# Performance work log

Hardware: AMD Instinct MI355X
Metric: run time of the kernel (lower is better)

The kernel has to match this reference:

```python
import jax, jax.numpy as jnp
import numpy as np

# Node feature layout used by gridfm-graphkit: [Pd, Qd, Pg, Qg, Vm, Va]
PD, QD, PG, QG, VM, VA = 0, 1, 2, 3, 4, 5

N_NODES = 2_000_000
N_EDGES = 32_000_000
N_FEAT = 6


def setup_inputs() -> dict:
    key = jax.random.key(0)
    k1, k2, k3, k4, k5 = jax.random.split(key, 5)
    pred = jax.random.normal(k1, (N_NODES, N_FEAT), dtype=jnp.float32)
    target = jax.random.normal(k2, (N_NODES, N_FEAT), dtype=jnp.float32)
    edge_attr = jax.random.normal(k3, (N_EDGES, 2), dtype=jnp.float32)  # (G, B)
    edge_index = jax.random.randint(k4, (2, N_EDGES), 0, N_NODES, dtype=jnp.int64)
    mask = jax.random.randint(k5, (N_NODES, N_FEAT), 0, 2) > 0  # True -> use prediction
    return {"pred": pred, "target": target, "edge_attr": edge_attr,
            "edge_index": edge_index, "mask": mask}


def _power_flow_residual(pred, target, edge_attr, edge_index, mask):
    # Use prediction where the value was masked, ground truth elsewhere.
    x = jnp.where(mask, pred, target)  # [N, 6]
    # Complex bus voltage V = Vm * exp(i Va)
    V = (x[:, VM] * jnp.exp(1j * x[:, VA])).astype(jnp.complex64)  # [N]
    # Complex admittance per edge (Ybus entry)
    Y = (edge_attr[:, 0] + 1j * edge_attr[:, 1]).astype(jnp.complex64)  # [E]
    src, dst = edge_index[0], edge_index[1]
    # PyG MessagePassing (source_to_target, aggr='add'):
    # I_i = sum_{e: dst(e)=i} Y_e * V_{src(e)}
    msgs = Y * V[src]  # [E] complex, gather on src
    I = jax.ops.segment_sum(msgs, dst, num_segments=pred.shape[0])  # [N] complex
    # Net injected complex power S = (Pg - Pd) + j (Qg - Qd)
    Sbus = (x[:, PG] - x[:, PD]) + 1j * (x[:, QG] - x[:, QD])
    # Power-flow residual: S - V * conj(I)
    return Sbus - V * jnp.conj(I)  # [N] complex64


def reference(pred, target, edge_attr, edge_index, mask):
    residual = _power_flow_residual(pred, target, edge_attr, edge_index, mask)
    loss = jnp.mean(jnp.abs(residual))
    real_loss = jnp.mean(jnp.abs(jnp.real(residual)))
    imag_loss = jnp.mean(jnp.abs(jnp.imag(residual)))
    # Matches {'loss', 'Active Power Loss', 'Reactive Power Loss'} of PBELoss
    return jnp.stack([loss, real_loss, imag_loss])
```

## Files before the change

### kernel.cpp

```cpp
#include <hip/hip_runtime.h>
#include <hip/hip_fp16.h>
#include <math.h>


#define PBE_NT     256
#define PBE_NB     512
#define PBE_BSHIFT 12
#define PBE_BSIZE  4096
#define PBE_TILE   4096
#define PBE_NTB    512
#define PBE_EPT    (PBE_TILE / PBE_NTB)

#define PBE_SCALE64       2097152.0f
#define PBE_INV_SCALE64   (1.0f / 2097152.0f)
#define PBE_SCALE_LDS     524288.0f
#define PBE_INV_SCALE_LDS (1.0f / 524288.0f)

typedef unsigned long long ull;
typedef int iv4 __attribute__((ext_vector_type(4)));
union H2U { __half2 h; unsigned u; };

__device__ __forceinline__ float2 ld_nt_f2(const float2* p) {
    double d = __builtin_nontemporal_load(reinterpret_cast<const double*>(p));
    union { double d; float2 f; } u; u.d = d;
    return u.f;
}
__device__ __forceinline__ int ld_nt_i(const int* p) {
    return __builtin_nontemporal_load(p);
}
__device__ __forceinline__ int2 ld_nt_i2(const int* p) {
    long long v = __builtin_nontemporal_load(reinterpret_cast<const long long*>(p));
    int2 r; r.x = (int)(unsigned)(v & 0xFFFFFFFFll); r.y = (int)(v >> 32);
    return r;
}
__device__ __forceinline__ iv4 ld_nt_iv4(const int* p) {
    return __builtin_nontemporal_load(reinterpret_cast<const iv4*>(p));
}

__global__ void pbe_node_prep(const float* __restrict__ pred,
                              const float* __restrict__ target,
                              const int* __restrict__ mask,
                              float* __restrict__ V,
                              float* __restrict__ S,
                              unsigned* __restrict__ Vh,
                              int n) {
    int i = blockIdx.x * blockDim.x + threadIdx.x;
    int stride = gridDim.x * blockDim.x;
    for (; i < n; i += stride) {
        int b = 6 * i;
        float2 p0 = ld_nt_f2((const float2*)(pred + b));
        float2 p1 = ld_nt_f2((const float2*)(pred + b + 2));
        float2 p2 = ld_nt_f2((const float2*)(pred + b + 4));
        float2 t0 = ld_nt_f2((const float2*)(target + b));
        float2 t1 = ld_nt_f2((const float2*)(target + b + 2));
        float2 t2 = ld_nt_f2((const float2*)(target + b + 4));
        int2 m0 = ld_nt_i2(mask + b);
        int2 m1 = ld_nt_i2(mask + b + 2);
        int2 m2 = ld_nt_i2(mask + b + 4);
        float pd = m0.x ? p0.x : t0.x;
        float qd = m0.y ? p0.y : t0.y;
        float pg = m1.x ? p1.x : t1.x;
        float qg = m1.y ? p1.y : t1.y;
        float vm = m2.x ? p2.x : t2.x;
        float va = m2.y ? p2.y : t2.y;
        float sn, cs;
        sincosf(va, &sn, &cs);
        float vr = vm * cs, vi = vm * sn;
        V[2 * i + 0] = vr;
        V[2 * i + 1] = vi;
        S[2 * i + 0] = pg - pd;
        S[2 * i + 1] = qg - qd;
        if (Vh) { H2U u; u.h = __floats2half2_rn(vr, vi); Vh[i] = u.u; }
    }
}

__global__ void pbe_hist(const int* __restrict__ dst,
                         unsigned* __restrict__ hist_g, int e_total) {
    __shared__ unsigned h[PBE_NB];
    for (int b = threadIdx.x; b < PBE_NB; b += blockDim.x) h[b] = 0;
    __syncthreads();
    int n4 = e_total >> 2;
    int i = blockIdx.x * blockDim.x + threadIdx.x;
    int stride = gridDim.x * blockDim.x;
    for (; i < n4; i += stride) {
        iv4 v = ld_nt_iv4(dst + 4 * i);
        atomicAdd(&h[((unsigned)v[0]) >> PBE_BSHIFT], 1u);
        atomicAdd(&h[((unsigned)v[1]) >> PBE_BSHIFT], 1u);
        atomicAdd(&h[((unsigned)v[2]) >> PBE_BSHIFT], 1u);
        atomicAdd(&h[((unsigned)v[3]) >> PBE_BSHIFT], 1u);
    }
    if (blockIdx.x == 0) {
        for (int t = (n4 << 2) + threadIdx.x; t < e_total; t += blockDim.x)
            atomicAdd(&h[((unsigned)dst[t]) >> PBE_BSHIFT], 1u);
    }
    __syncthreads();
    for (int b = threadIdx.x; b < PBE_NB; b += blockDim.x)
        if (h[b]) atomicAdd(&hist_g[b], h[b]);
}

__global__ void pbe_prefix(const unsigned* __restrict__ hist_g,
                           unsigned* __restrict__ base,
                           unsigned* __restrict__ cursor) {
    __shared__ unsigned tmp[PBE_NB];
    int t = threadIdx.x;
    unsigned mine = hist_g[t];
    tmp[t] = mine;
    __syncthreads();
    for (int o = 1; o < PBE_NB; o <<= 1) {
        unsigned u = (t >= o) ? tmp[t - o] : 0u;
        __syncthreads();
        tmp[t] += u;
        __syncthreads();
    }
    unsigned excl = tmp[t] - mine;
    base[t] = excl;
    cursor[t] = excl;
}

__global__ void __launch_bounds__(PBE_NTB)
pbe_bin(const float2* __restrict__ Y,
        const int* __restrict__ src,
        const int* __restrict__ dst,
        const unsigned* __restrict__ Vh,
        ull* __restrict__ rec,
        unsigned* __restrict__ cursor,
        int e_total) {
    __shared__ unsigned hist[PBE_NB];
    __shared__ unsigned lbase[PBE_NB];
    __shared__ unsigned wsum[8];
    __shared__ unsigned staged_sh;
    __shared__ ull recs[PBE_TILE];

    const int tile0 = blockIdx.x * PBE_TILE;
    const int tid = threadIdx.x;
    hist[tid] = 0;
    __syncthreads();

    int d[PBE_EPT];
    #pragma unroll
    for (int k = 0; k < PBE_EPT; ++k) {
        int i = tile0 + k * PBE_NTB + tid;
        d[k] = (i < e_total) ? ld_nt_i(dst + i) : -1;
    }
    #pragma unroll
    for (int k = 0; k < PBE_EPT; ++k)
        if (d[k] >= 0) atomicAdd(&hist[((unsigned)d[k]) >> PBE_BSHIFT], 1u);
    __syncthreads();

    {
        unsigned mine = hist[tid];
        unsigned v = mine;
        #pragma unroll
        for (int o = 1; o < 64; o <<= 1) {
            unsigned u = __shfl_up(v, o);
            if ((tid & 63) >= o) v += u;
        }
        if ((tid & 63) == 63) wsum[tid >> 6] = v;
        __syncthreads();
        if (tid == 0) {
            unsigned acc = 0;
            #pragma unroll
            for (int wv = 0; wv < 8; ++wv) {
                unsigned t = wsum[wv]; wsum[wv] = acc; acc += t;
            }
        }
        __syncthreads();
        unsigned incl = v + wsum[tid >> 6];
        unsigned excl = incl - mine;
        lbase[tid] = excl;
        if (tid == PBE_NB - 1) staged_sh = incl;
        unsigned g = mine ? atomicAdd(&cursor[tid], mine) : 0u;
        hist[tid] = g - excl;
    }
    __syncthreads();

    #pragma unroll
    for (int h = 0; h < PBE_EPT / 8; ++h) {
        int s8[8]; unsigned uv[8]; float2 y8[8];
        #pragma unroll
        for (int j = 0; j < 8; ++j) {
            int k = h * 8 + j;
            int i = tile0 + k * PBE_NTB + tid;
            s8[j] = (d[k] >= 0) ? ld_nt_i(src + i) : 0;
        }
        #pragma unroll
        for (int j = 0; j < 8; ++j) uv[j] = Vh[s8[j]];
        #pragma unroll
        for (int j = 0; j < 8; ++j) {
            int k = h * 8 + j;
            int i = tile0 + k * PBE_NTB + tid;
            y8[j] = (d[k] >= 0) ? ld_nt_f2(Y + i) : make_float2(0.f, 0.f);
        }
        #pragma unroll
        for (int j = 0; j < 8; ++j) {
            int k = h * 8 + j;
            if (d[k] < 0) continue;
            unsigned b = ((unsigned)d[k]) >> PBE_BSHIFT;
            unsigned pos = atomicAdd(&lbase[b], 1u);
            H2U uvh; uvh.u = uv[j];
            float vr = __low2float(uvh.h), vi = __high2float(uvh.h);
            float mr = y8[j].x * vr - y8[j].y * vi;
            float mi = y8[j].x * vi + y8[j].y * vr;
            H2U um; um.h = __floats2half2_rn(mr, mi);
            recs[pos] = ((ull)b << 44)
                      | ((ull)(unsigned)(d[k] & (PBE_BSIZE - 1)) << 32)
                      | um.u;
        }
    }
    __syncthreads();

    unsigned staged = staged_sh;
    for (unsigned j = tid; j < staged; j += PBE_NTB) {
        ull r = recs[j];
        unsigned b = (unsigned)(r >> 44);
        __builtin_nontemporal_store(r & 0xFFFFFFFFFFFull, &rec[j + hist[b]]);
    }
}

__global__ void __launch_bounds__(512)
pbe_bucket_acc_red(const ull* __restrict__ rec,
                   const unsigned* __restrict__ base,
                   const unsigned* __restrict__ cursor,
                   const float* __restrict__ V,
                   const float* __restrict__ S,
                   float* __restrict__ sums, int n_nodes) {
    __shared__ int accR[PBE_BSIZE];
    __shared__ int accI[PBE_BSIZE];
    for (int j = threadIdx.x; j < PBE_BSIZE; j += 512) { accR[j] = 0; accI[j] = 0; }
    __syncthreads();
    const int b = blockIdx.x;
    const unsigned lo = base[b], hi = cursor[b];
    for (unsigned t = lo + threadIdx.x; t < hi; t += 512) {
        ull p = __builtin_nontemporal_load(rec + t);
        H2U um; um.u = (unsigned)p;
        unsigned dl = (unsigned)(p >> 32) & (PBE_BSIZE - 1);
        atomicAdd(&accR[dl], __float2int_rn(__low2float(um.h) * PBE_SCALE_LDS));
        atomicAdd(&accI[dl], __float2int_rn(__high2float(um.h) * PBE_SCALE_LDS));
    }
    __syncthreads();
    const int node0 = b << PBE_BSHIFT;
    float a0 = 0.f, a1 = 0.f, a2 = 0.f;
    for (int j = threadIdx.x; j < PBE_BSIZE; j += 512) {
        int n = node0 + j;
        if (n < n_nodes) {
            float2 v  = reinterpret_cast<const float2*>(V)[n];
            float2 sb = reinterpret_cast<const float2*>(S)[n];
            float cr = accR[j] * PBE_INV_SCALE_LDS;
            float ci = accI[j] * PBE_INV_SCALE_LDS;
            float rr = sb.x - (v.x * cr + v.y * ci);
            float ri = sb.y - (v.y * cr - v.x * ci);
            a0 += sqrtf(rr * rr + ri * ri);
            a1 += fabsf(rr);
            a2 += fabsf(ri);
        }
    }
    #pragma unroll
    for (int off = 32; off > 0; off >>= 1) {
        a0 += __shfl_down(a0, off);
        a1 += __shfl_down(a1, off);
        a2 += __shfl_down(a2, off);
    }
    __shared__ float sm[3][8];
    int wid  = threadIdx.x >> 6;
    int lane = threadIdx.x & 63;
    if (lane == 0) { sm[0][wid] = a0; sm[1][wid] = a1; sm[2][wid] = a2; }
    __syncthreads();
    if (threadIdx.x == 0) {
        float t0 = 0.f, t1 = 0.f, t2 = 0.f;
        #pragma unroll
        for (int wv = 0; wv < 8; ++wv) {
            t0 += sm[0][wv]; t1 += sm[1][wv]; t2 += sm[2][wv];
        }
        atomicAdd(&sums[0], t0);
        atomicAdd(&sums[1], t1);
        atomicAdd(&sums[2], t2);
    }
}

__device__ __forceinline__ void pbe_edge_one(float2 gb, int s, int d,
                                             const float2* __restrict__ V,
                                             ull* __restrict__ Iq) {
    float2 v = V[s];
    float mr = gb.x * v.x - gb.y * v.y;
    float mi = gb.x * v.y + gb.y * v.x;
    int qr = __float2int_rn(mr * PBE_SCALE64);
    int qi = __float2int_rn(mi * PBE_SCALE64);
    ull pack = ((ull)(unsigned)qr << 32) + (ull)(long long)qi;
    atomicAdd(&Iq[d], pack);
}

__global__ void __launch_bounds__(PBE_NT)
pbe_edge_scatter(const float2* __restrict__ edge_attr,
                 const int* __restrict__ src,
                 const int* __restrict__ dst,
                 const float2* __restrict__ V,
                 ull* __restrict__ Iq,
                 int e_total) {
    int i = blockIdx.x * blockDim.x + threadIdx.x;
    const int stride = gridDim.x * blockDim.x;
    for (; i + 3 * stride < e_total; i += 4 * stride) {
        int ia = i, ib = i + stride, ic = i + 2 * stride, id = i + 3 * stride;
        float2 ga = ld_nt_f2(edge_attr + ia);
        float2 gb = ld_nt_f2(edge_attr + ib);
        float2 gc = ld_nt_f2(edge_attr + ic);
        float2 gd = ld_nt_f2(edge_attr + id);
        int sa = ld_nt_i(src + ia), sb = ld_nt_i(src + ib);
        int sc = ld_nt_i(src + ic), sd = ld_nt_i(src + id);
        int da = ld_nt_i(dst + ia), db = ld_nt_i(dst + ib);
        int dc = ld_nt_i(dst + ic), dd = ld_nt_i(dst + id);
        pbe_edge_one(ga, sa, da, V, Iq);
        pbe_edge_one(gb, sb, db, V, Iq);
        pbe_edge_one(gc, sc, dc, V, Iq);
        pbe_edge_one(gd, sd, dd, V, Iq);
    }
    for (; i < e_total; i += stride) {
        float2 g = ld_nt_f2(edge_attr + i);
        pbe_edge_one(g, ld_nt_i(src + i), ld_nt_i(dst + i), V, Iq);
    }
}

__global__ void pbe_unpack_iq(ull* __restrict__ Iq, float* __restrict__ I, int n) {
    int i = blockIdx.x * blockDim.x + threadIdx.x;
    int stride = gridDim.x * blockDim.x;
    for (; i < n; i += stride) {
        long long q = (long long)Iq[i];
        int lo = (int)(unsigned)(q & 0xFFFFFFFFll);
        int hi = (int)((q - (long long)lo) >> 32);
        I[2 * i + 0] = hi * PBE_INV_SCALE64;
        I[2 * i + 1] = lo * PBE_INV_SCALE64;
    }
}

__global__ void pbe_reduce(const float* __restrict__ V,
                           const float* __restrict__ S,
                           const float* __restrict__ I,
                           float* __restrict__ sums, int n) {
    float a0 = 0.f, a1 = 0.f, a2 = 0.f;
    int i = blockIdx.x * blockDim.x + threadIdx.x;
    int stride = gridDim.x * blockDim.x;
    for (; i < n; i += stride) {
        float2 v  = reinterpret_cast<const float2*>(V)[i];
        float2 sb = reinterpret_cast<const float2*>(S)[i];
        float2 cc = reinterpret_cast<const float2*>(I)[i];
        float rr = sb.x - (v.x * cc.x + v.y * cc.y);
        float ri = sb.y - (v.y * cc.x - v.x * cc.y);
        a0 += sqrtf(rr * rr + ri * ri);
        a1 += fabsf(rr);
        a2 += fabsf(ri);
    }
    #pragma unroll
    for (int off = 32; off > 0; off >>= 1) {
        a0 += __shfl_down(a0, off);
        a1 += __shfl_down(a1, off);
        a2 += __shfl_down(a2, off);
    }
    __shared__ float sm[3][PBE_NT / 64];
    int wid  = threadIdx.x >> 6;
    int lane = threadIdx.x & 63;
    if (lane == 0) { sm[0][wid] = a0; sm[1][wid] = a1; sm[2][wid] = a2; }
    __syncthreads();
    if (threadIdx.x == 0) {
        float t0 = 0.f, t1 = 0.f, t2 = 0.f;
        #pragma unroll
        for (int w = 0; w < PBE_NT / 64; ++w) {
            t0 += sm[0][w]; t1 += sm[1][w]; t2 += sm[2][w];
        }
        atomicAdd(&sums[0], t0);
        atomicAdd(&sums[1], t1);
        atomicAdd(&sums[2], t2);
    }
}

__global__ void pbe_finalize(const float* __restrict__ sums,
                             float* __restrict__ out, float inv_n) {
    int t = threadIdx.x;
    if (t < 3) out[t] = sums[t] * inv_n;
}

static inline size_t align256(size_t x) { return (x + 255) & ~(size_t)255; }

extern "C" void kernel_launch(void* const* d_in, const int* in_sizes, int n_in,
                              void* d_out, int out_size, void* d_ws, size_t ws_size,
                              hipStream_t stream) {
    const float* pred      = (const float*)d_in[0];
    const float* target    = (const float*)d_in[1];
    const float* edge_attr = (const float*)d_in[2];
    const int*   edge_idx  = (const int*)d_in[3];
    const int*   mask      = (const int*)d_in[4];

    const int n_nodes = in_sizes[0] / 6;
    const int n_edges = in_sizes[2] / 2;
    const int* src = edge_idx;
    const int* dst = edge_idx + n_edges;

    const int NBa     = (n_nodes + PBE_BSIZE - 1) / PBE_BSIZE;
    const int n_tiles = (n_edges + PBE_TILE - 1) / PBE_TILE;

    char* w = (char*)d_ws;
    size_t oV    = 0;
    size_t oS    = align256(oV + (size_t)2 * n_nodes * 4);
    size_t oVh   = align256(oS + (size_t)2 * n_nodes * 4);
    size_t oRec  = align256(oVh + (size_t)n_nodes * 4);
    size_t oHist = align256(oRec + (size_t)n_edges * 8);
    size_t oBase = align256(oHist + PBE_NB * 4);
    size_t oCur  = align256(oBase + PBE_NB * 4);
    size_t oSums = align256(oCur + PBE_NB * 4);
    size_t need  = oSums + 3 * 4;

    float*    V      = (float*)(w + oV);
    float*    S      = (float*)(w + oS);
    unsigned* Vh     = (unsigned*)(w + oVh);
    ull*      rec    = (ull*)(w + oRec);
    unsigned* hist_g = (unsigned*)(w + oHist);
    unsigned* base   = (unsigned*)(w + oBase);
    unsigned* cursor = (unsigned*)(w + oCur);
    float*    sums   = (float*)(w + oSums);

    const bool fast = (ws_size >= need) && (NBa <= PBE_NB);

    const int T = PBE_NT;
    int grid_nodes = (n_nodes + T - 1) / T;
    if (grid_nodes > 4096) grid_nodes = 4096;

    if (fast) {
        hipMemsetAsync(hist_g, 0, PBE_NB * sizeof(unsigned), stream);
        hipMemsetAsync(sums, 0, 3 * sizeof(float), stream);

        pbe_node_prep<<<grid_nodes, T, 0, stream>>>(pred, target, mask, V, S, Vh, n_nodes);
        pbe_hist<<<1024, T, 0, stream>>>(dst, hist_g, n_edges);
        pbe_prefix<<<1, PBE_NB, 0, stream>>>(hist_g, base, cursor);
        pbe_bin<<<n_tiles, PBE_NTB, 0, stream>>>((const float2*)edge_attr, src, dst,
                                                 Vh, rec, cursor, n_edges);
        pbe_bucket_acc_red<<<NBa, 512, 0, stream>>>(rec, base, cursor, V, S,
                                                    sums, n_nodes);
        pbe_finalize<<<1, 64, 0, stream>>>(sums, (float*)d_out, 1.0f / (float)n_nodes);
    } else {
        ull* Iq = (ull*)(w + oRec);
        float* sums_fb = (float*)(w + oVh);
        hipMemsetAsync(Iq, 0, (size_t)n_nodes * 8, stream);
        hipMemsetAsync(sums_fb, 0, 3 * sizeof(float), stream);
        int grid_edges = (n_edges + T - 1) / T;
        if (grid_edges > 8192) grid_edges = 8192;
        pbe_node_prep<<<grid_nodes, T, 0, stream>>>(pred, target, mask, V, S,
                                                    (unsigned*)nullptr, n_nodes);
        pbe_edge_scatter<<<grid_edges, T, 0, stream>>>(
            (const float2*)edge_attr, src, dst, (const float2*)V, Iq, n_edges);
        pbe_unpack_iq<<<grid_nodes, T, 0, stream>>>(Iq, (float*)Iq, n_nodes);
        pbe_reduce<<<grid_nodes, T, 0, stream>>>(V, S, (float*)Iq, sums_fb, n_nodes);
        pbe_finalize<<<1, 64, 0, stream>>>(sums_fb, (float*)d_out, 1.0f / (float)n_nodes);
    }
}
```

Before: 672.3 us.

## Fuse node prep with dst histogram and vectorize per-thread contiguous edge loads in binning

```diff
diff --git a/kernel.cpp b/kernel.cpp
--- a/kernel.cpp
+++ b/kernel.cpp
@@ -9,7 +9,7 @@
 #define PBE_BSIZE  4096
 #define PBE_TILE   4096
 #define PBE_NTB    512
-#define PBE_EPT    (PBE_TILE / PBE_NTB)
+#define PBE_EPT    8
 
 #define PBE_SCALE64       2097152.0f
 #define PBE_INV_SCALE64   (1.0f / 2097152.0f)
@@ -17,7 +17,8 @@
 #define PBE_INV_SCALE_LDS (1.0f / 524288.0f)
 
 typedef unsigned long long ull;
-typedef int iv4 __attribute__((ext_vector_type(4)));
+typedef int   iv4 __attribute__((ext_vector_type(4)));
+typedef float fv4 __attribute__((ext_vector_type(4)));
 union H2U { __half2 h; unsigned u; };
 
 __device__ __forceinline__ float2 ld_nt_f2(const float2* p) {
@@ -36,17 +37,26 @@
 __device__ __forceinline__ iv4 ld_nt_iv4(const int* p) {
     return __builtin_nontemporal_load(reinterpret_cast<const iv4*>(p));
 }
-
-__global__ void pbe_node_prep(const float* __restrict__ pred,
+__device__ __forceinline__ fv4 ld_nt_fv4(const float* p) {
+    return __builtin_nontemporal_load(reinterpret_cast<const fv4*>(p));
+}
+
+__global__ void pbe_prep_hist(const float* __restrict__ pred,
                               const float* __restrict__ target,
                               const int* __restrict__ mask,
                               float* __restrict__ V,
                               float* __restrict__ S,
                               unsigned* __restrict__ Vh,
-                              int n) {
-    int i = blockIdx.x * blockDim.x + threadIdx.x;
+                              int n,
+                              const int* __restrict__ dst,
+                              unsigned* __restrict__ hist_g,
+                              int e_total) {
+    __shared__ unsigned h[PBE_NB];
+    for (int b = threadIdx.x; b < PBE_NB; b += blockDim.x) h[b] = 0;
+    __syncthreads();
+    int gtid = blockIdx.x * blockDim.x + threadIdx.x;
     int stride = gridDim.x * blockDim.x;
-    for (; i < n; i += stride) {
+    for (int i = gtid; i < n; i += stride) {
         int b = 6 * i;
         float2 p0 = ld_nt_f2((const float2*)(pred + b));
         float2 p1 = ld_nt_f2((const float2*)(pred + b + 2));
@@ -70,19 +80,10 @@
         V[2 * i + 1] = vi;
         S[2 * i + 0] = pg - pd;
         S[2 * i + 1] = qg - qd;
-        if (Vh) { H2U u; u.h = __floats2half2_rn(vr, vi); Vh[i] = u.u; }
-    }
-}
-
-__global__ void pbe_hist(const int* __restrict__ dst,
-                         unsigned* __restrict__ hist_g, int e_total) {
-    __shared__ unsigned h[PBE_NB];
-    for (int b = threadIdx.x; b < PBE_NB; b += blockDim.x) h[b] = 0;
-    __syncthreads();
+        H2U u; u.h = __floats2half2_rn(vr, vi); Vh[i] = u.u;
+    }
     int n4 = e_total >> 2;
-    int i = blockIdx.x * blockDim.x + threadIdx.x;
-    int stride = gridDim.x * blockDim.x;
-    for (; i < n4; i += stride) {
+    for (int i = gtid; i < n4; i += stride) {
         iv4 v = ld_nt_iv4(dst + 4 * i);
         atomicAdd(&h[((unsigned)v[0]) >> PBE_BSHIFT], 1u);
         atomicAdd(&h[((unsigned)v[1]) >> PBE_BSHIFT], 1u);
@@ -118,7 +119,7 @@
 }
 
 __global__ void __launch_bounds__(PBE_NTB)
-pbe_bin(const float2* __restrict__ Y,
+pbe_bin(const float* __restrict__ Y,
         const int* __restrict__ src,
         const int* __restrict__ dst,
         const unsigned* __restrict__ Vh,
@@ -136,11 +137,19 @@
     hist[tid] = 0;
     __syncthreads();
 
+    const int ebase = tile0 + tid * PBE_EPT;
+    const bool full = (tile0 + PBE_TILE) <= e_total;
+
     int d[PBE_EPT];
-    #pragma unroll
-    for (int k = 0; k < PBE_EPT; ++k) {
-        int i = tile0 + k * PBE_NTB + tid;
-        d[k] = (i < e_total) ? ld_nt_i(dst + i) : -1;
+    if (full) {
+        iv4 a = ld_nt_iv4(dst + ebase);
+        iv4 b = ld_nt_iv4(dst + ebase + 4);
+        d[0]=a[0]; d[1]=a[1]; d[2]=a[2]; d[3]=a[3];
+        d[4]=b[0]; d[5]=b[1]; d[6]=b[2]; d[7]=b[3];
+    } else {
+        #pragma unroll
+        for (int j = 0; j < PBE_EPT; ++j)
+            d[j] = (ebase + j < e_total) ? dst[ebase + j] : -1;
     }
     #pragma unroll
     for (int k = 0; k < PBE_EPT; ++k)
@@ -174,36 +183,41 @@
     }
     __syncthreads();
 
-    #pragma unroll
-    for (int h = 0; h < PBE_EPT / 8; ++h) {
-        int s8[8]; unsigned uv[8]; float2 y8[8];
-        #pragma unroll
-        for (int j = 0; j < 8; ++j) {
-            int k = h * 8 + j;
-            int i = tile0 + k * PBE_NTB + tid;
-            s8[j] = (d[k] >= 0) ? ld_nt_i(src + i) : 0;
-        }
-        #pragma unroll
-        for (int j = 0; j < 8; ++j) uv[j] = Vh[s8[j]];
-        #pragma unroll
-        for (int j = 0; j < 8; ++j) {
-            int k = h * 8 + j;
-            int i = tile0 + k * PBE_NTB + tid;
-            y8[j] = (d[k] >= 0) ? ld_nt_f2(Y + i) : make_float2(0.f, 0.f);
-        }
-        #pragma unroll
-        for (int j = 0; j < 8; ++j) {
-            int k = h * 8 + j;
-            if (d[k] < 0) continue;
-            unsigned b = ((unsigned)d[k]) >> PBE_BSHIFT;
+    {
+        int s[PBE_EPT]; float2 y[PBE_EPT]; unsigned uv[PBE_EPT];
+        if (full) {
+            iv4 a = ld_nt_iv4(src + ebase);
+            iv4 b = ld_nt_iv4(src + ebase + 4);
+            s[0]=a[0]; s[1]=a[1]; s[2]=a[2]; s[3]=a[3];
+            s[4]=b[0]; s[5]=b[1]; s[6]=b[2]; s[7]=b[3];
+            #pragma unroll
+            for (int m = 0; m < 4; ++m) {
+                fv4 q = ld_nt_fv4(Y + 2 * (ebase + 2 * m));
+                y[2*m+0] = make_float2(q[0], q[1]);
+                y[2*m+1] = make_float2(q[2], q[3]);
+            }
+        } else {
+            #pragma unroll
+            for (int j = 0; j < PBE_EPT; ++j) {
+                s[j] = (d[j] >= 0) ? src[ebase + j] : 0;
+                y[j] = (d[j] >= 0) ? *(const float2*)(Y + 2 * (ebase + j))
+                                   : make_float2(0.f, 0.f);
+            }
+        }
+        #pragma unroll
+        for (int j = 0; j < PBE_EPT; ++j) uv[j] = Vh[s[j]];
+        #pragma unroll
+        for (int j = 0; j < PBE_EPT; ++j) {
+            if (d[j] < 0) continue;
+            unsigned b = ((unsigned)d[j]) >> PBE_BSHIFT;
             unsigned pos = atomicAdd(&lbase[b], 1u);
             H2U uvh; uvh.u = uv[j];
             float vr = __low2float(uvh.h), vi = __high2float(uvh.h);
-            float mr = y8[j].x * vr - y8[j].y * vi;
-            float mi = y8[j].x * vi + y8[j].y * vr;
+            float mr = y[j].x * vr - y[j].y * vi;
+            float mi = y[j].x * vi + y[j].y * vr;
             H2U um; um.h = __floats2half2_rn(mr, mi);
             recs[pos] = ((ull)b << 44)
-                      | ((ull)(unsigned)(d[k] & (PBE_BSIZE - 1)) << 32)
+                      | ((ull)(unsigned)(d[j] & (PBE_BSIZE - 1)) << 32)
                       | um.u;
         }
     }
@@ -277,6 +291,40 @@
     }
 }
 
+__global__ void pbe_node_prep(const float* __restrict__ pred,
+                              const float* __restrict__ target,
+                              const int* __restrict__ mask,
+                              float* __restrict__ V,
+                              float* __restrict__ S,
+                              int n) {
+    int i = blockIdx.x * blockDim.x + threadIdx.x;
+    int stride = gridDim.x * blockDim.x;
+    for (; i < n; i += stride) {
+        int b = 6 * i;
+        float2 p0 = ld_nt_f2((const float2*)(pred + b));
+        float2 p1 = ld_nt_f2((const float2*)(pred + b + 2));
+        float2 p2 = ld_nt_f2((const float2*)(pred + b + 4));
+        float2 t0 = ld_nt_f2((const float2*)(target + b));
+        float2 t1 = ld_nt_f2((const float2*)(target + b + 2));
+        float2 t2 = ld_nt_f2((const float2*)(target + b + 4));
+        int2 m0 = ld_nt_i2(mask + b);
+        int2 m1 = ld_nt_i2(mask + b + 2);
+        int2 m2 = ld_nt_i2(mask + b + 4);
+        float pd = m0.x ? p0.x : t0.x;
+        float qd = m0.y ? p0.y : t0.y;
+        float pg = m1.x ? p1.x : t1.x;
+        float qg = m1.y ? p1.y : t1.y;
+        float vm = m2.x ? p2.x : t2.x;
+        float va = m2.y ? p2.y : t2.y;
+        float sn, cs;
+        sincosf(va, &sn, &cs);
+        V[2 * i + 0] = vm * cs;
+        V[2 * i + 1] = vm * sn;
+        S[2 * i + 0] = pg - pd;
+        S[2 * i + 1] = qg - qd;
+    }
+}
+
 __device__ __forceinline__ void pbe_edge_one(float2 gb, int s, int d,
                                              const float2* __restrict__ V,
                                              ull* __restrict__ Iq) {
@@ -298,21 +346,6 @@
                  int e_total) {
     int i = blockIdx.x * blockDim.x + threadIdx.x;
     const int stride = gridDim.x * blockDim.x;
-    for (; i + 3 * stride < e_total; i += 4 * stride) {
-        int ia = i, ib = i + stride, ic = i + 2 * stride, id = i + 3 * stride;
-        float2 ga = ld_nt_f2(edge_attr + ia);
-        float2 gb = ld_nt_f2(edge_attr + ib);
-        float2 gc = ld_nt_f2(edge_attr + ic);
-        float2 gd = ld_nt_f2(edge_attr + id);
-        int sa = ld_nt_i(src + ia), sb = ld_nt_i(src + ib);
-        int sc = ld_nt_i(src + ic), sd = ld_nt_i(src + id);
-        int da = ld_nt_i(dst + ia), db = ld_nt_i(dst + ib);
-        int dc = ld_nt_i(dst + ic), dd = ld_nt_i(dst + id);
-        pbe_edge_one(ga, sa, da, V, Iq);
-        pbe_edge_one(gb, sb, db, V, Iq);
-        pbe_edge_one(gc, sc, dc, V, Iq);
-        pbe_edge_one(gd, sd, dd, V, Iq);
-    }
     for (; i < e_total; i += stride) {
         float2 g = ld_nt_f2(edge_attr + i);
         pbe_edge_one(g, ld_nt_i(src + i), ld_nt_i(dst + i), V, Iq);
@@ -420,17 +453,17 @@
 
     const int T = PBE_NT;
     int grid_nodes = (n_nodes + T - 1) / T;
-    if (grid_nodes > 4096) grid_nodes = 4096;
+    if (grid_nodes > 2048) grid_nodes = 2048;
 
     if (fast) {
         hipMemsetAsync(hist_g, 0, PBE_NB * sizeof(unsigned), stream);
         hipMemsetAsync(sums, 0, 3 * sizeof(float), stream);
 
-        pbe_node_prep<<<grid_nodes, T, 0, stream>>>(pred, target, mask, V, S, Vh, n_nodes);
-        pbe_hist<<<1024, T, 0, stream>>>(dst, hist_g, n_edges);
+        pbe_prep_hist<<<2048, T, 0, stream>>>(pred, target, mask, V, S, Vh,
+                                              n_nodes, dst, hist_g, n_edges);
         pbe_prefix<<<1, PBE_NB, 0, stream>>>(hist_g, base, cursor);
-        pbe_bin<<<n_tiles, PBE_NTB, 0, stream>>>((const float2*)edge_attr, src, dst,
-                                                 Vh, rec, cursor, n_edges);
+        pbe_bin<<<n_tiles, PBE_NTB, 0, stream>>>(edge_attr, src, dst, Vh,
+                                                 rec, cursor, n_edges);
         pbe_bucket_acc_red<<<NBa, 512, 0, stream>>>(rec, base, cursor, V, S,
                                                     sums, n_nodes);
         pbe_finalize<<<1, 64, 0, stream>>>(sums, (float*)d_out, 1.0f / (float)n_nodes);
@@ -441,8 +474,7 @@
         hipMemsetAsync(sums_fb, 0, 3 * sizeof(float), stream);
         int grid_edges = (n_edges + T - 1) / T;
         if (grid_edges > 8192) grid_edges = 8192;
-        pbe_node_prep<<<grid_nodes, T, 0, stream>>>(pred, target, mask, V, S,
-                                                    (unsigned*)nullptr, n_nodes);
+        pbe_node_prep<<<grid_nodes, T, 0, stream>>>(pred, target, mask, V, S, n_nodes);
         pbe_edge_scatter<<<grid_edges, T, 0, stream>>>(
             (const float2*)edge_attr, src, dst, (const float2*)V, Iq, n_edges);
         pbe_unpack_iq<<<grid_nodes, T, 0, stream>>>(Iq, (float*)Iq, n_nodes);
```

Measured after the change: 691.9 us. 1.03x slower.
